# Kernel optimization log

Measured on AMD Instinct MI355X. Metric: run time of the kernel, lower is better.

Reference implementation:

```python
import jax, jax.numpy as jnp
import numpy as np

B, LAT, ADIM, NACT, H = 131072, 64, 16, 9, 128

def setup_inputs() -> dict:
    key = jax.random.key(0)
    ks = jax.random.split(key, 24)
    p = lambda k, shp: (jax.random.normal(k, shp, dtype=jnp.float32) * 0.05)
    return {
        "z_t": jax.random.normal(ks[0], (B, LAT), dtype=jnp.float32),
        "action": jax.random.randint(ks[1], (B,), 0, NACT),
        "hidden": jnp.zeros((1, B, H), dtype=jnp.float32),
        "embed": p(ks[2], (NACT, ADIM)),
        "fuse_W": p(ks[3], (H, LAT + ADIM)), "fuse_b": p(ks[4], (H,)),
        "W_ih": p(ks[5], (3 * H, H)), "W_hh": p(ks[6], (3 * H, H)),
        "b_ih": p(ks[7], (3 * H,)), "b_hh": p(ks[8], (3 * H,)),
        "ns_W1": p(ks[9], (H, H)), "ns_b1": p(ks[10], (H,)),
        "ns_W2": p(ks[11], (LAT, H)), "ns_b2": p(ks[12], (LAT,)),
        "rw_W1": p(ks[13], (H // 2, H)), "rw_b1": p(ks[14], (H // 2,)),
        "rw_W2": p(ks[15], (1, H // 2)), "rw_b2": p(ks[16], (1,)),
        "dn_W1": p(ks[17], (H // 2, H)), "dn_b1": p(ks[18], (H // 2,)),
        "dn_W2": p(ks[19], (1, H // 2)), "dn_b2": p(ks[20], (1,)),
    }

def _mlp2(x, W1, b1, W2, b2):
    return jax.nn.relu(x @ W1.T + b1) @ W2.T + b2

def reference(z_t, action, hidden, embed, fuse_W, fuse_b, W_ih, W_hh, b_ih, b_hh,
              ns_W1, ns_b1, ns_W2, ns_b2, rw_W1, rw_b1, rw_W2, rw_b2,
              dn_W1, dn_b1, dn_W2, dn_b2):
    a_emb = embed[action]                                  # [B, ADIM]
    fused = jnp.concatenate([z_t, a_emb], axis=-1)         # [B, LAT+ADIM]
    x = jax.nn.relu(fused @ fuse_W.T + fuse_b)             # [B, H]
    h0 = hidden[0]                                         # [B, H]
    gi = x @ W_ih.T + b_ih                                 # [B, 3H]
    gh = h0 @ W_hh.T + b_hh                                # [B, 3H]
    Hd = x.shape[-1]
    r = jax.nn.sigmoid(gi[:, :Hd] + gh[:, :Hd])
    zg = jax.nn.sigmoid(gi[:, Hd:2 * Hd] + gh[:, Hd:2 * Hd])
    n = jnp.tanh(gi[:, 2 * Hd:] + r * gh[:, 2 * Hd:])
    h_new = (1.0 - zg) * n + zg * h0                       # [B, H]
    out = h_new
    z_next = _mlp2(out, ns_W1, ns_b1, ns_W2, ns_b2)        # [B, LAT]
    reward = _mlp2(out, rw_W1, rw_b1, rw_W2, rw_b2)        # [B, 1]
    done_logit = _mlp2(out, dn_W1, dn_b1, dn_W2, dn_b2)    # [B, 1]
    return (z_next, reward, done_logit, h_new[None])
```

## Files before the change

### kernel.cpp

```cpp
#include <hip/hip_runtime.h>
#include <cstddef>
#include <cstdint>

#define BATCH 131072
#define HOFF ((size_t)BATCH * 66)

typedef __attribute__((ext_vector_type(8))) short short8;
typedef __attribute__((ext_vector_type(4))) short short4v;
typedef __attribute__((ext_vector_type(4))) float f32x4;

typedef const __attribute__((address_space(1))) unsigned int* gas_t;
typedef __attribute__((address_space(3))) unsigned int* las_t;

#define WS_WF    0
#define WS_GRU   13312
#define WS_HEAD  119808
#define WS_ELEMS 165888

#define MFMA(a,b,c) __builtin_amdgcn_mfma_f32_16x16x32_bf16((a),(b),(c),0,0,0)

__device__ __forceinline__ short f2bf(float x) {
    unsigned u = __builtin_bit_cast(unsigned, x);
    unsigned r = (u + 0x7fffu + ((u >> 16) & 1u)) >> 16;
    return (short)r;
}
__device__ __forceinline__ float bf2f(short s) {
    unsigned u = ((unsigned)(unsigned short)s) << 16;
    return __builtin_bit_cast(float, u);
}
__device__ __forceinline__ float fsigmoid(float x) { return __builtin_amdgcn_rcpf(1.0f + __expf(-x)); }
__device__ __forceinline__ float ftanh(float x)    { return 1.0f - 2.0f * __builtin_amdgcn_rcpf(1.0f + __expf(2.0f * x)); }

__device__ __forceinline__ short8 packbf(f32x4 a, f32x4 b) {
    short8 r;
    r[0]=f2bf(a[0]); r[1]=f2bf(a[1]); r[2]=f2bf(a[2]); r[3]=f2bf(a[3]);
    r[4]=f2bf(b[0]); r[5]=f2bf(b[1]); r[6]=f2bf(b[2]); r[7]=f2bf(b[3]);
    return r;
}

template<int NCH>
__device__ __forceinline__ void stage_lds(const short* __restrict__ src, short* dst, int t) {
    constexpr int NP = (NCH + 255) / 256;
    #pragma unroll
    for (int k = 0; k < NP; ++k) {
        int c = t + 256 * k;
        if ((NCH % 256 == 0) || c < NCH)
            __builtin_amdgcn_global_load_lds((gas_t)(const void*)(src + (size_t)c * 8),
                                             (las_t)(void*)(dst + (size_t)c * 8), 16, 0, 0);
    }
}

extern "C" __global__ void prep_weights(const float* __restrict__ fuse_W,
                                        const float* __restrict__ W_ih, const float* __restrict__ W_hh,
                                        const float* __restrict__ ns_W1, const float* __restrict__ ns_W2,
                                        const float* __restrict__ rw_W1, const float* __restrict__ dn_W1,
                                        short* __restrict__ ws) {
    int i = blockIdx.x * 256 + threadIdx.x;
    if (i >= WS_ELEMS) return;
    float v = 0.f;
    if (i < WS_GRU) {
        int j = i / 104, k = i % 104;
        if (k < 80) v = fuse_W[j*80 + k];
    } else if (i < WS_HEAD) {
        int g = (i - WS_GRU) / 6656, e = (i - WS_GRU) % 6656;
        int r = e / 136, k = e % 136;
        if (r < 48 && k < 128) {
            int j = g >> 1;
            const float* W = (g & 1) ? W_hh : W_ih;
            int gate = r >> 4, rr = r & 15;
            v = W[(size_t)(gate*128 + j*16 + rr)*128 + k];
        }
    } else {
        int h = (i - WS_HEAD) / 4608, e = (i - WS_HEAD) % 4608;
        int r = e / 136, k = e % 136;
        if (r < 32 && k < 128) {
            const float* W; int rb;
            if (h < 4)      { W = ns_W1; rb = h*32; }
            else if (h < 6) { W = ns_W2; rb = (h-4)*32; }
            else if (h < 8) { W = rw_W1; rb = (h-6)*32; }
            else            { W = dn_W1; rb = (h-8)*32; }
            v = W[(size_t)(rb + r)*128 + k];
        }
    }
    ws[i] = f2bf(v);
}

extern "C" __global__ __launch_bounds__(256, 2)
void gru_mfma(const float* __restrict__ z_t, const int* __restrict__ action,
              const float* __restrict__ hidden, const float* __restrict__ embed,
              const float* __restrict__ fuse_b,
              const float* __restrict__ b_ih, const float* __restrict__ b_hh,
              const float* __restrict__ ns_b1, const float* __restrict__ ns_b2,
              const float* __restrict__ rw_b1, const float* __restrict__ rw_W2, const float* __restrict__ rw_b2,
              const float* __restrict__ dn_b1, const float* __restrict__ dn_W2, const float* __restrict__ dn_b2,
              const short* __restrict__ ws, float* __restrict__ out)
{
    __shared__ __align__(16) short smem[30720];

    const int t    = threadIdx.x;
    const int lane = t & 63;
    const int w    = t >> 6;
    const int lo   = lane & 15;
    const int hi   = lane >> 4;
    const int R    = blockIdx.x * 128 + w * 32;
    short* const aw = &smem[13312 + w * 4352];

    const f32x4 zz4 = {0.f, 0.f, 0.f, 0.f};

    stage_lds<1664>(ws, &smem[0], t);

    short8 fa[2][3];
    short8 ha[2][4];
    #pragma unroll
    for (int rt = 0; rt < 2; ++rt) {
        const int row = R + rt*16 + lo;
        #pragma unroll
        for (int kt = 0; kt < 2; ++kt) {
            f32x4 p0 = *(const f32x4*)&z_t[(size_t)row*64 + kt*32 + hi*8];
            f32x4 p1 = *(const f32x4*)&z_t[(size_t)row*64 + kt*32 + hi*8 + 4];
            fa[rt][kt] = packbf(p0, p1);
        }
        if (hi < 2) {
            int a = action[row];
            f32x4 e0 = *(const f32x4*)&embed[a*16 + hi*8];
            f32x4 e1 = *(const f32x4*)&embed[a*16 + hi*8 + 4];
            fa[rt][2] = packbf(e0, e1);
        } else {
            short8 z8 = {0,0,0,0,0,0,0,0};
            fa[rt][2] = z8;
        }
        #pragma unroll
        for (int kt = 0; kt < 4; ++kt) {
            f32x4 p0 = *(const f32x4*)&hidden[(size_t)row*128 + kt*32 + hi*8];
            f32x4 p1 = *(const f32x4*)&hidden[(size_t)row*128 + kt*32 + hi*8 + 4];
            ha[rt][kt] = packbf(p0, p1);
        }
    }

    #pragma unroll
    for (int rt = 0; rt < 2; ++rt)
        #pragma unroll
        for (int kt = 0; kt < 4; ++kt)
            *(short8*)&aw[(rt*16 + lo)*136 + kt*32 + hi*8] = ha[rt][kt];
    unsigned h0d[8][2][2];
    #pragma unroll
    for (int j = 0; j < 8; ++j)
        #pragma unroll
        for (int rt = 0; rt < 2; ++rt)
            #pragma unroll
            for (int p = 0; p < 2; ++p) {
                unsigned a = (unsigned short)aw[(rt*16 + 4*hi + 2*p    )*136 + j*16 + lo];
                unsigned b = (unsigned short)aw[(rt*16 + 4*hi + 2*p + 1)*136 + j*16 + lo];
                h0d[j][rt][p] = a | (b << 16);
            }
    __syncthreads();

    #pragma unroll 1
    for (int ct = 0; ct < 8; ++ct) {
        float fb = fuse_b[ct*16 + lo];
        f32x4 a0 = zz4, a1 = zz4;
        #pragma unroll
        for (int kt = 0; kt < 3; ++kt) {
            short8 B = *(const short8*)&smem[(ct*16 + lo)*104 + kt*32 + hi*8];
            a0 = MFMA(fa[0][kt], B, a0);
            a1 = MFMA(fa[1][kt], B, a1);
        }
        #pragma unroll
        for (int e = 0; e < 4; ++e) {
            aw[(4*hi + e)*136 + ct*16 + lo]        = f2bf(fmaxf(a0[e] + fb, 0.f));
            aw[(16 + 4*hi + e)*136 + ct*16 + lo]   = f2bf(fmaxf(a1[e] + fb, 0.f));
        }
    }
    short8 xa[2][4];
    #pragma unroll
    for (int rt = 0; rt < 2; ++rt)
        #pragma unroll
        for (int kt = 0; kt < 4; ++kt)
            xa[rt][kt] = *(const short8*)&aw[(rt*16 + lo)*136 + kt*32 + hi*8];

    __syncthreads();
    stage_lds<832>(ws + WS_GRU, &smem[0], t);
    __syncthreads();

    f32x4 accI[3][2], accH[3][2];
    #pragma unroll
    for (int j = 0; j < 8; ++j) {
        stage_lds<832>(ws + WS_GRU + (size_t)(2*j + 1) * 6656, &smem[6656], t);
        #pragma unroll
        for (int g = 0; g < 3; ++g) {
            accI[g][0] = zz4; accI[g][1] = zz4;
            #pragma unroll
            for (int kt = 0; kt < 4; ++kt) {
                short8 B = *(const short8*)&smem[(g*16 + lo)*136 + kt*32 + hi*8];
                accI[g][0] = MFMA(xa[0][kt], B, accI[g][0]);
                accI[g][1] = MFMA(xa[1][kt], B, accI[g][1]);
            }
        }
        __syncthreads();

        if (j < 7) stage_lds<832>(ws + WS_GRU + (size_t)(2*j + 2) * 6656, &smem[0], t);
        else       stage_lds<576>(ws + WS_HEAD, &smem[0], t);
        #pragma unroll
        for (int g = 0; g < 3; ++g) {
            accH[g][0] = zz4; accH[g][1] = zz4;
            #pragma unroll
            for (int kt = 0; kt < 4; ++kt) {
                short8 B = *(const short8*)&smem[6656 + (g*16 + lo)*136 + kt*32 + hi*8];
                accH[g][0] = MFMA(ha[0][kt], B, accH[g][0]);
                accH[g][1] = MFMA(ha[1][kt], B, accH[g][1]);
            }
        }
        {
            const int j0 = j * 16;
            const float bir = b_ih[j0+lo], biz = b_ih[128+j0+lo], bin = b_ih[256+j0+lo];
            const float bhr = b_hh[j0+lo], bhz = b_hh[128+j0+lo], bhn = b_hh[256+j0+lo];
            #pragma unroll
            for (int rt = 0; rt < 2; ++rt) {
                #pragma unroll
                for (int p = 0; p < 2; ++p) {
                    unsigned hp = h0d[j][rt][p];
                    float h0a = bf2f((short)(hp & 0xffffu));
                    float h0b = bf2f((short)(hp >> 16));
                    int e = 2*p;
                    {
                        float rg = fsigmoid(accI[0][rt][e] + bir + accH[0][rt][e] + bhr);
                        float zg = fsigmoid(accI[1][rt][e] + biz + accH[1][rt][e] + bhz);
                        float ng = ftanh(accI[2][rt][e] + bin + rg*(accH[2][rt][e] + bhn));
                        aw[(rt*16 + 4*hi + e)*136 + j0 + lo] = f2bf((1.f - zg)*ng + zg*h0a);
                    }
                    {
                        float rg = fsigmoid(accI[0][rt][e+1] + bir + accH[0][rt][e+1] + bhr);
                        float zg = fsigmoid(accI[1][rt][e+1] + biz + accH[1][rt][e+1] + bhz);
                        float ng = ftanh(accI[2][rt][e+1] + bin + rg*(accH[2][rt][e+1] + bhn));
                        aw[(rt*16 + 4*hi + e+1)*136 + j0 + lo] = f2bf((1.f - zg)*ng + zg*h0b);
                    }
                }
            }
        }
        __syncthreads();
    }

    short8 hfa[2][4], ta[2][4];
    #pragma unroll 1
    for (int u = 16; u < 26; ++u) {
        if (u < 25)
            stage_lds<576>(ws + WS_HEAD + (size_t)(u - 15) * 4608, &smem[((u+1)&1)*6656], t);
        const int halfB = (u & 1) * 6656;

        if (u == 16) {
            #pragma unroll 1
            for (int i = 0; i < 16; ++i) {
                int v = i*64 + lane;
                int row = v >> 5, col = (v & 31) * 4;
                short4v s = *(const short4v*)&aw[row*136 + col];
                f32x4 f = { bf2f(s[0]), bf2f(s[1]), bf2f(s[2]), bf2f(s[3]) };
                *(f32x4*)&out[HOFF + (size_t)(R + row)*128 + col] = f;
            }
            #pragma unroll
            for (int rt = 0; rt < 2; ++rt)
                #pragma unroll
                for (int kt = 0; kt < 4; ++kt)
                    hfa[rt][kt] = *(const short8*)&aw[(rt*16 + lo)*136 + kt*32 + hi*8];
        }
        if (u == 20) {
            #pragma unroll
            for (int rt = 0; rt < 2; ++rt)
                #pragma unroll
                for (int kt = 0; kt < 4; ++kt)
                    ta[rt][kt] = *(const short8*)&aw[(rt*16 + lo)*136 + kt*32 + hi*8];
        }

        if (u < 20) {
            const int uh = u - 16;
            #pragma unroll
            for (int sub = 0; sub < 2; ++sub) {
                const int j0 = (uh*2 + sub) * 16;
                float b1 = ns_b1[j0 + lo];
                f32x4 a0 = zz4, a1 = zz4;
                #pragma unroll
                for (int kt = 0; kt < 4; ++kt) {
                    short8 B = *(const short8*)&smem[halfB + (sub*16 + lo)*136 + kt*32 + hi*8];
                    a0 = MFMA(hfa[0][kt], B, a0);
                    a1 = MFMA(hfa[1][kt], B, a1);
                }
                #pragma unroll
                for (int e = 0; e < 4; ++e) {
                    aw[(4*hi + e)*136 + j0 + lo]      = f2bf(fmaxf(a0[e] + b1, 0.f));
                    aw[(16 + 4*hi + e)*136 + j0 + lo] = f2bf(fmaxf(a1[e] + b1, 0.f));
                }
            }
        } else if (u < 22) {
            const int uh = u - 20;
            #pragma unroll
            for (int sub = 0; sub < 2; ++sub) {
                const int j0 = (uh*2 + sub) * 16;
                float b2 = ns_b2[j0 + lo];
                f32x4 a0 = zz4, a1 = zz4;
                #pragma unroll
                for (int kt = 0; kt < 4; ++kt) {
                    short8 B = *(const short8*)&smem[halfB + (sub*16 + lo)*136 + kt*32 + hi*8];
                    a0 = MFMA(ta[0][kt], B, a0);
                    a1 = MFMA(ta[1][kt], B, a1);
                }
                #pragma unroll
                for (int e = 0; e < 4; ++e) {
                    aw[(4*hi + e)*72 + j0 + lo]      = f2bf(a0[e] + b2);
                    aw[(16 + 4*hi + e)*72 + j0 + lo] = f2bf(a1[e] + b2);
                }
            }
            if (u == 21) {
                #pragma unroll 1
                for (int i = 0; i < 8; ++i) {
                    int v = i*64 + lane;
                    int row = v >> 4, col = (v & 15) * 4;
                    short4v s = *(const short4v*)&aw[row*72 + col];
                    f32x4 f = { bf2f(s[0]), bf2f(s[1]), bf2f(s[2]), bf2f(s[3]) };
                    *(f32x4*)&out[(size_t)(R + row)*64 + col] = f;
                }
            }
        } else if (u < 24) {
            const int uh = u - 22;
            #pragma unroll
            for (int sub = 0; sub < 2; ++sub) {
                const int j0 = (uh*2 + sub) * 16;
                float b1 = rw_b1[j0 + lo];
                f32x4 a0 = zz4, a1 = zz4;
                #pragma unroll
                for (int kt = 0; kt < 4; ++kt) {
                    short8 B = *(const short8*)&smem[halfB + (sub*16 + lo)*136 + kt*32 + hi*8];
                    a0 = MFMA(hfa[0][kt], B, a0);
                    a1 = MFMA(hfa[1][kt], B, a1);
                }
                #pragma unroll
                for (int e = 0; e < 4; ++e) {
                    aw[(4*hi + e)*136 + j0 + lo]      = f2bf(fmaxf(a0[e] + b1, 0.f));
                    aw[(16 + 4*hi + e)*136 + j0 + lo] = f2bf(fmaxf(a1[e] + b1, 0.f));
                }
            }
        } else {
            const int uh = u - 24;
            #pragma unroll
            for (int sub = 0; sub < 2; ++sub) {
                const int j0 = (uh*2 + sub) * 16;
                float b1 = dn_b1[j0 + lo];
                f32x4 a0 = zz4, a1 = zz4;
                #pragma unroll
                for (int kt = 0; kt < 4; ++kt) {
                    short8 B = *(const short8*)&smem[halfB + (sub*16 + lo)*136 + kt*32 + hi*8];
                    a0 = MFMA(hfa[0][kt], B, a0);
                    a1 = MFMA(hfa[1][kt], B, a1);
                }
                #pragma unroll
                for (int e = 0; e < 4; ++e) {
                    aw[(4*hi + e)*136 + 64 + j0 + lo]      = f2bf(fmaxf(a0[e] + b1, 0.f));
                    aw[(16 + 4*hi + e)*136 + 64 + j0 + lo] = f2bf(fmaxf(a1[e] + b1, 0.f));
                }
            }
        }
        __syncthreads();
    }

    {
        const float* W2   = (lane < 32) ? rw_W2 : dn_W2;
        float acc         = (lane < 32) ? rw_b2[0] : dn_b2[0];
        const int colbase = (lane < 32) ? 0 : 64;
        const int rr      = lane & 31;
        #pragma unroll
        for (int k = 0; k < 64; k += 4) {
            short4v s = *(const short4v*)&aw[rr*136 + colbase + k];
            f32x4 wv  = *(const f32x4*)&W2[k];
            acc += bf2f(s[0])*wv[0] + bf2f(s[1])*wv[1] + bf2f(s[2])*wv[2] + bf2f(s[3])*wv[3];
        }
        size_t ooff = (lane < 32) ? ((size_t)BATCH*64) : ((size_t)BATCH*65);
        out[ooff + R + rr] = acc;
    }
}

extern "C" void kernel_launch(void* const* d_in, const int* in_sizes, int n_in,
                              void* d_out, int out_size, void* d_ws, size_t ws_size,
                              hipStream_t stream) {
    const float* z_t    = (const float*)d_in[0];
    const int*   action = (const int*)  d_in[1];
    const float* hidden = (const float*)d_in[2];
    const float* embed  = (const float*)d_in[3];
    const float* fuse_W = (const float*)d_in[4];
    const float* fuse_b = (const float*)d_in[5];
    const float* W_ih   = (const float*)d_in[6];
    const float* W_hh   = (const float*)d_in[7];
    const float* b_ih   = (const float*)d_in[8];
    const float* b_hh   = (const float*)d_in[9];
    const float* ns_W1  = (const float*)d_in[10];
    const float* ns_b1  = (const float*)d_in[11];
    const float* ns_W2  = (const float*)d_in[12];
    const float* ns_b2  = (const float*)d_in[13];
    const float* rw_W1  = (const float*)d_in[14];
    const float* rw_b1  = (const float*)d_in[15];
    const float* rw_W2  = (const float*)d_in[16];
    const float* rw_b2  = (const float*)d_in[17];
    const float* dn_W1  = (const float*)d_in[18];
    const float* dn_b1  = (const float*)d_in[19];
    const float* dn_W2  = (const float*)d_in[20];
    const float* dn_b2  = (const float*)d_in[21];
    float* out = (float*)d_out;
    short* ws  = (short*)d_ws;

    hipLaunchKernelGGL(prep_weights, dim3((WS_ELEMS + 255) / 256), dim3(256), 0, stream,
                       fuse_W, W_ih, W_hh, ns_W1, ns_W2, rw_W1, dn_W1, ws);

    hipLaunchKernelGGL(gru_mfma, dim3(BATCH / 128), dim3(256), 0, stream,
                       z_t, action, hidden, embed,
                       fuse_b, b_ih, b_hh, ns_b1, ns_b2,
                       rw_b1, rw_W2, rw_b2, dn_b1, dn_W2, dn_b2,
                       ws, out);
}
```

Measured before the change: 92.99 us.

## Double block size, shrink per-wave LDS scratch, and interleave output stores with compute

Blocks grow from 256 to 512 threads (8 waves, 256 rows), and launch bounds request 4 blocks per CU. Each wave's LDS scratch shrinks from a 136-wide row buffer to two 40-wide strip buffers, so more waves fit and each staged weight tile serves more rows. Stores of h_new are spread across the GRU loop, the fuse layer is split so weight staging overlaps compute, and the head stage loop is unrolled into explicit steps with the scalar heads computed from strips. The cost is higher register pressure under the tighter launch bound, and two of the h_new fragments are reloaded from global output memory.

After: 128.3 us. 1.38x slower.

```diff
diff --git a/kernel.cpp b/kernel.cpp
--- a/kernel.cpp
+++ b/kernel.cpp
@@ -12,7 +12,6 @@
 typedef const __attribute__((address_space(1))) unsigned int* gas_t;
 typedef __attribute__((address_space(3))) unsigned int* las_t;
 
-#define WS_WF    0
 #define WS_GRU   13312
 #define WS_HEAD  119808
 #define WS_ELEMS 165888
@@ -40,11 +39,11 @@
 
 template<int NCH>
 __device__ __forceinline__ void stage_lds(const short* __restrict__ src, short* dst, int t) {
-    constexpr int NP = (NCH + 255) / 256;
+    constexpr int NP = (NCH + 511) / 512;
     #pragma unroll
     for (int k = 0; k < NP; ++k) {
-        int c = t + 256 * k;
-        if ((NCH % 256 == 0) || c < NCH)
+        int c = t + 512 * k;
+        if ((NCH % 512 == 0) || c < NCH)
             __builtin_amdgcn_global_load_lds((gas_t)(const void*)(src + (size_t)c * 8),
                                              (las_t)(void*)(dst + (size_t)c * 8), 16, 0, 0);
     }
@@ -85,7 +84,25 @@
     ws[i] = f2bf(v);
 }
 
-extern "C" __global__ __launch_bounds__(256, 2)
+#define HEAD_GEMM(FRAG, BIAS, Q, HALFOFF, SP, RELU) do {                                   \
+    _Pragma("unroll") for (int sub = 0; sub < 2; ++sub) {                                  \
+        float bb = (BIAS)[(Q)*32 + sub*16 + lo];                                           \
+        f32x4 a0 = zz4, a1 = zz4;                                                          \
+        _Pragma("unroll") for (int kt = 0; kt < 4; ++kt) {                                 \
+            short8 Bf = *(const short8*)&smem[(HALFOFF) + (sub*16+lo)*136 + kt*32 + hi*8]; \
+            a0 = MFMA((FRAG)[0][kt], Bf, a0); a1 = MFMA((FRAG)[1][kt], Bf, a1); }          \
+        _Pragma("unroll") for (int e = 0; e < 4; ++e) {                                    \
+            float v0 = a0[e] + bb, v1 = a1[e] + bb;                                        \
+            if (RELU) { v0 = fmaxf(v0, 0.f); v1 = fmaxf(v1, 0.f); }                        \
+            (SP)[(4*hi+e)*40 + sub*16 + lo]      = f2bf(v0);                               \
+            (SP)[(16+4*hi+e)*40 + sub*16 + lo]   = f2bf(v1); }                             \
+    } } while (0)
+
+#define TA_READ(Q, SP) do {                                            \
+    ta[0][Q] = *(const short8*)&(SP)[lo*40 + hi*8];                    \
+    ta[1][Q] = *(const short8*)&(SP)[(16+lo)*40 + hi*8]; } while (0)
+
+extern "C" __global__ __launch_bounds__(512, 4)
 void gru_mfma(const float* __restrict__ z_t, const int* __restrict__ action,
               const float* __restrict__ hidden, const float* __restrict__ embed,
               const float* __restrict__ fuse_b,
@@ -93,19 +110,55 @@
               const float* __restrict__ ns_b1, const float* __restrict__ ns_b2,
               const float* __restrict__ rw_b1, const float* __restrict__ rw_W2, const float* __restrict__ rw_b2,
               const float* __restrict__ dn_b1, const float* __restrict__ dn_W2, const float* __restrict__ dn_b2,
-              const short* __restrict__ ws, float* __restrict__ out)
+              const short* __restrict__ ws, float* out)
 {
-    __shared__ __align__(16) short smem[30720];
+    __shared__ __align__(16) short smem[33792];
 
     const int t    = threadIdx.x;
     const int lane = t & 63;
     const int w    = t >> 6;
     const int lo   = lane & 15;
     const int hi   = lane >> 4;
-    const int R    = blockIdx.x * 128 + w * 32;
-    short* const aw = &smem[13312 + w * 4352];
+    const int R    = blockIdx.x * 256 + w * 32;
+    short* const S0 = &smem[13312 + w * 2560];
+    short* const S1 = S0 + 1280;
 
     const f32x4 zz4 = {0.f, 0.f, 0.f, 0.f};
+
+    auto store_hnew_strip = [&](const short* SP, int kt) {
+        #pragma unroll
+        for (int v = 0; v < 4; ++v) {
+            int idx = v*64 + lane;
+            int r = idx >> 3, c = (idx & 7) * 4;
+            short4v s = *(const short4v*)&SP[r*40 + c];
+            f32x4 f = { bf2f(s[0]), bf2f(s[1]), bf2f(s[2]), bf2f(s[3]) };
+            *(f32x4*)&out[HOFF + (size_t)(R + r)*128 + kt*32 + c] = f;
+        }
+    };
+    auto store_z_strip = [&](const short* SP, int q) {
+        #pragma unroll
+        for (int v = 0; v < 4; ++v) {
+            int idx = v*64 + lane;
+            int r = idx >> 3, c = (idx & 7) * 4;
+            short4v s = *(const short4v*)&SP[r*40 + c];
+            f32x4 f = { bf2f(s[0]), bf2f(s[1]), bf2f(s[2]), bf2f(s[3]) };
+            *(f32x4*)&out[(size_t)(R + r)*64 + q*32 + c] = f;
+        }
+    };
+    auto head1_dot = [&](const float* W2, float b2) -> float {
+        int rr = lane & 31;
+        float acc = b2;
+        #pragma unroll
+        for (int kk = 0; kk < 64; kk += 8) {
+            const short* SP = (kk < 32) ? S0 : S1;
+            short8 s = *(const short8*)&SP[rr*40 + (kk & 31)];
+            f32x4 w0 = *(const f32x4*)&W2[kk];
+            f32x4 w1 = *(const f32x4*)&W2[kk+4];
+            acc += bf2f(s[0])*w0[0] + bf2f(s[1])*w0[1] + bf2f(s[2])*w0[2] + bf2f(s[3])*w0[3]
+                 + bf2f(s[4])*w1[0] + bf2f(s[5])*w1[1] + bf2f(s[6])*w1[2] + bf2f(s[7])*w1[3];
+        }
+        return acc;
+    };
 
     stage_lds<1664>(ws, &smem[0], t);
 
@@ -136,56 +189,90 @@
             ha[rt][kt] = packbf(p0, p1);
         }
     }
-
-    #pragma unroll
-    for (int rt = 0; rt < 2; ++rt)
-        #pragma unroll
-        for (int kt = 0; kt < 4; ++kt)
-            *(short8*)&aw[(rt*16 + lo)*136 + kt*32 + hi*8] = ha[rt][kt];
+    float fbv[8];
+    #pragma unroll
+    for (int ct = 0; ct < 8; ++ct) fbv[ct] = fuse_b[ct*16 + lo];
+
     unsigned h0d[8][2][2];
     #pragma unroll
-    for (int j = 0; j < 8; ++j)
-        #pragma unroll
-        for (int rt = 0; rt < 2; ++rt)
-            #pragma unroll
-            for (int p = 0; p < 2; ++p) {
-                unsigned a = (unsigned short)aw[(rt*16 + 4*hi + 2*p    )*136 + j*16 + lo];
-                unsigned b = (unsigned short)aw[(rt*16 + 4*hi + 2*p + 1)*136 + j*16 + lo];
-                h0d[j][rt][p] = a | (b << 16);
-            }
-    __syncthreads();
-
-    #pragma unroll 1
-    for (int ct = 0; ct < 8; ++ct) {
-        float fb = fuse_b[ct*16 + lo];
-        f32x4 a0 = zz4, a1 = zz4;
-        #pragma unroll
-        for (int kt = 0; kt < 3; ++kt) {
-            short8 B = *(const short8*)&smem[(ct*16 + lo)*104 + kt*32 + hi*8];
-            a0 = MFMA(fa[0][kt], B, a0);
-            a1 = MFMA(fa[1][kt], B, a1);
-        }
-        #pragma unroll
-        for (int e = 0; e < 4; ++e) {
-            aw[(4*hi + e)*136 + ct*16 + lo]        = f2bf(fmaxf(a0[e] + fb, 0.f));
-            aw[(16 + 4*hi + e)*136 + ct*16 + lo]   = f2bf(fmaxf(a1[e] + fb, 0.f));
-        }
-    }
+    for (int kt = 0; kt < 4; ++kt) {
+        short* SP = (kt & 1) ? S1 : S0;
+        *(short8*)&SP[lo*40 + hi*8]        = ha[0][kt];
+        *(short8*)&SP[(16 + lo)*40 + hi*8] = ha[1][kt];
+        #pragma unroll
+        for (int c = 0; c < 2; ++c) {
+            int j = 2*kt + c;
+            #pragma unroll
+            for (int rt = 0; rt < 2; ++rt)
+                #pragma unroll
+                for (int p = 0; p < 2; ++p) {
+                    unsigned a = (unsigned short)SP[(rt*16 + 4*hi + 2*p    )*40 + c*16 + lo];
+                    unsigned b = (unsigned short)SP[(rt*16 + 4*hi + 2*p + 1)*40 + c*16 + lo];
+                    h0d[j][rt][p] = a | (b << 16);
+                }
+        }
+    }
+    __syncthreads();
+
     short8 xa[2][4];
     #pragma unroll
-    for (int rt = 0; rt < 2; ++rt)
-        #pragma unroll
-        for (int kt = 0; kt < 4; ++kt)
-            xa[rt][kt] = *(const short8*)&aw[(rt*16 + lo)*136 + kt*32 + hi*8];
-
+    for (int kt = 0; kt < 2; ++kt) {
+        short* SP = (kt & 1) ? S1 : S0;
+        #pragma unroll
+        for (int c = 0; c < 2; ++c) {
+            int ct = kt*2 + c;
+            f32x4 a0 = zz4, a1 = zz4;
+            #pragma unroll
+            for (int fk = 0; fk < 3; ++fk) {
+                short8 B = *(const short8*)&smem[(ct*16 + lo)*104 + fk*32 + hi*8];
+                a0 = MFMA(fa[0][fk], B, a0);
+                a1 = MFMA(fa[1][fk], B, a1);
+            }
+            #pragma unroll
+            for (int e = 0; e < 4; ++e) {
+                SP[(4*hi + e)*40 + c*16 + lo]      = f2bf(fmaxf(a0[e] + fbv[ct], 0.f));
+                SP[(16 + 4*hi + e)*40 + c*16 + lo] = f2bf(fmaxf(a1[e] + fbv[ct], 0.f));
+            }
+        }
+        xa[0][kt] = *(const short8*)&SP[lo*40 + hi*8];
+        xa[1][kt] = *(const short8*)&SP[(16 + lo)*40 + hi*8];
+    }
     __syncthreads();
     stage_lds<832>(ws + WS_GRU, &smem[0], t);
-    __syncthreads();
-
-    f32x4 accI[3][2], accH[3][2];
+
+    #pragma unroll
+    for (int kt = 2; kt < 4; ++kt) {
+        short* SP = (kt & 1) ? S1 : S0;
+        #pragma unroll
+        for (int c = 0; c < 2; ++c) {
+            int ct = kt*2 + c;
+            f32x4 a0 = zz4, a1 = zz4;
+            #pragma unroll
+            for (int fk = 0; fk < 3; ++fk) {
+                short8 B = *(const short8*)&smem[6656 + ((ct - 4)*16 + lo)*104 + fk*32 + hi*8];
+                a0 = MFMA(fa[0][fk], B, a0);
+                a1 = MFMA(fa[1][fk], B, a1);
+            }
+            #pragma unroll
+            for (int e = 0; e < 4; ++e) {
+                SP[(4*hi + e)*40 + c*16 + lo]      = f2bf(fmaxf(a0[e] + fbv[ct], 0.f));
+                SP[(16 + 4*hi + e)*40 + c*16 + lo] = f2bf(fmaxf(a1[e] + fbv[ct], 0.f));
+            }
+        }
+        xa[0][kt] = *(const short8*)&SP[lo*40 + hi*8];
+        xa[1][kt] = *(const short8*)&SP[(16 + lo)*40 + hi*8];
+    }
+    __syncthreads();
+
     #pragma unroll
     for (int j = 0; j < 8; ++j) {
-        stage_lds<832>(ws + WS_GRU + (size_t)(2*j + 1) * 6656, &smem[6656], t);
+        stage_lds<832>(ws + WS_GRU + (size_t)(2*j + 1)*6656, &smem[6656], t);
+        if (j == 2) store_hnew_strip(S0, 0);
+        if (j == 4) store_hnew_strip(S1, 1);
+        const int j0 = j * 16;
+        const float bir = b_ih[j0+lo], biz = b_ih[128+j0+lo], bin = b_ih[256+j0+lo];
+        const float bhr = b_hh[j0+lo], bhz = b_hh[128+j0+lo], bhn = b_hh[256+j0+lo];
+        f32x4 accI[3][2];
         #pragma unroll
         for (int g = 0; g < 3; ++g) {
             accI[g][0] = zz4; accI[g][1] = zz4;
@@ -198,8 +285,9 @@
         }
         __syncthreads();
 
-        if (j < 7) stage_lds<832>(ws + WS_GRU + (size_t)(2*j + 2) * 6656, &smem[0], t);
+        if (j < 7) stage_lds<832>(ws + WS_GRU + (size_t)(2*j + 2)*6656, &smem[0], t);
         else       stage_lds<576>(ws + WS_HEAD, &smem[0], t);
+        f32x4 accH[3][2];
         #pragma unroll
         for (int g = 0; g < 3; ++g) {
             accH[g][0] = zz4; accH[g][1] = zz4;
@@ -211,9 +299,7 @@
             }
         }
         {
-            const int j0 = j * 16;
-            const float bir = b_ih[j0+lo], biz = b_ih[128+j0+lo], bin = b_ih[256+j0+lo];
-            const float bhr = b_hh[j0+lo], bhz = b_hh[128+j0+lo], bhn = b_hh[256+j0+lo];
+            short* HP = ((j >> 1) & 1) ? S1 : S0;
             #pragma unroll
             for (int rt = 0; rt < 2; ++rt) {
                 #pragma unroll
@@ -226,13 +312,13 @@
                         float rg = fsigmoid(accI[0][rt][e] + bir + accH[0][rt][e] + bhr);
                         float zg = fsigmoid(accI[1][rt][e] + biz + accH[1][rt][e] + bhz);
                         float ng = ftanh(accI[2][rt][e] + bin + rg*(accH[2][rt][e] + bhn));
-                        aw[(rt*16 + 4*hi + e)*136 + j0 + lo] = f2bf((1.f - zg)*ng + zg*h0a);
+                        HP[(rt*16 + 4*hi + e)*40 + (j&1)*16 + lo] = f2bf((1.f - zg)*ng + zg*h0a);
                     }
                     {
                         float rg = fsigmoid(accI[0][rt][e+1] + bir + accH[0][rt][e+1] + bhr);
                         float zg = fsigmoid(accI[1][rt][e+1] + biz + accH[1][rt][e+1] + bhz);
                         float ng = ftanh(accI[2][rt][e+1] + bin + rg*(accH[2][rt][e+1] + bhn));
-                        aw[(rt*16 + 4*hi + e+1)*136 + j0 + lo] = f2bf((1.f - zg)*ng + zg*h0b);
+                        HP[(rt*16 + 4*hi + e+1)*40 + (j&1)*16 + lo] = f2bf((1.f - zg)*ng + zg*h0b);
                     }
                 }
             }
@@ -241,138 +327,72 @@
     }
 
     short8 hfa[2][4], ta[2][4];
-    #pragma unroll 1
-    for (int u = 16; u < 26; ++u) {
-        if (u < 25)
-            stage_lds<576>(ws + WS_HEAD + (size_t)(u - 15) * 4608, &smem[((u+1)&1)*6656], t);
-        const int halfB = (u & 1) * 6656;
-
-        if (u == 16) {
-            #pragma unroll 1
-            for (int i = 0; i < 16; ++i) {
-                int v = i*64 + lane;
-                int row = v >> 5, col = (v & 31) * 4;
-                short4v s = *(const short4v*)&aw[row*136 + col];
-                f32x4 f = { bf2f(s[0]), bf2f(s[1]), bf2f(s[2]), bf2f(s[3]) };
-                *(f32x4*)&out[HOFF + (size_t)(R + row)*128 + col] = f;
-            }
-            #pragma unroll
-            for (int rt = 0; rt < 2; ++rt)
-                #pragma unroll
-                for (int kt = 0; kt < 4; ++kt)
-                    hfa[rt][kt] = *(const short8*)&aw[(rt*16 + lo)*136 + kt*32 + hi*8];
-        }
-        if (u == 20) {
-            #pragma unroll
-            for (int rt = 0; rt < 2; ++rt)
-                #pragma unroll
-                for (int kt = 0; kt < 4; ++kt)
-                    ta[rt][kt] = *(const short8*)&aw[(rt*16 + lo)*136 + kt*32 + hi*8];
-        }
-
-        if (u < 20) {
-            const int uh = u - 16;
-            #pragma unroll
-            for (int sub = 0; sub < 2; ++sub) {
-                const int j0 = (uh*2 + sub) * 16;
-                float b1 = ns_b1[j0 + lo];
-                f32x4 a0 = zz4, a1 = zz4;
-                #pragma unroll
-                for (int kt = 0; kt < 4; ++kt) {
-                    short8 B = *(const short8*)&smem[halfB + (sub*16 + lo)*136 + kt*32 + hi*8];
-                    a0 = MFMA(hfa[0][kt], B, a0);
-                    a1 = MFMA(hfa[1][kt], B, a1);
-                }
-                #pragma unroll
-                for (int e = 0; e < 4; ++e) {
-                    aw[(4*hi + e)*136 + j0 + lo]      = f2bf(fmaxf(a0[e] + b1, 0.f));
-                    aw[(16 + 4*hi + e)*136 + j0 + lo] = f2bf(fmaxf(a1[e] + b1, 0.f));
-                }
-            }
-        } else if (u < 22) {
-            const int uh = u - 20;
-            #pragma unroll
-            for (int sub = 0; sub < 2; ++sub) {
-                const int j0 = (uh*2 + sub) * 16;
-                float b2 = ns_b2[j0 + lo];
-                f32x4 a0 = zz4, a1 = zz4;
-                #pragma unroll
-                for (int kt = 0; kt < 4; ++kt) {
-                    short8 B = *(const short8*)&smem[halfB + (sub*16 + lo)*136 + kt*32 + hi*8];
-                    a0 = MFMA(ta[0][kt], B, a0);
-                    a1 = MFMA(ta[1][kt], B, a1);
-                }
-                #pragma unroll
-                for (int e = 0; e < 4; ++e) {
-                    aw[(4*hi + e)*72 + j0 + lo]      = f2bf(a0[e] + b2);
-                    aw[(16 + 4*hi + e)*72 + j0 + lo] = f2bf(a1[e] + b2);
-                }
-            }
-            if (u == 21) {
-                #pragma unroll 1
-                for (int i = 0; i < 8; ++i) {
-                    int v = i*64 + lane;
-                    int row = v >> 4, col = (v & 15) * 4;
-                    short4v s = *(const short4v*)&aw[row*72 + col];
-                    f32x4 f = { bf2f(s[0]), bf2f(s[1]), bf2f(s[2]), bf2f(s[3]) };
-                    *(f32x4*)&out[(size_t)(R + row)*64 + col] = f;
-                }
-            }
-        } else if (u < 24) {
-            const int uh = u - 22;
-            #pragma unroll
-            for (int sub = 0; sub < 2; ++sub) {
-                const int j0 = (uh*2 + sub) * 16;
-                float b1 = rw_b1[j0 + lo];
-                f32x4 a0 = zz4, a1 = zz4;
-                #pragma unroll
-                for (int kt = 0; kt < 4; ++kt) {
-                    short8 B = *(const short8*)&smem[halfB + (sub*16 + lo)*136 + kt*32 + hi*8];
-                    a0 = MFMA(hfa[0][kt], B, a0);
-                    a1 = MFMA(hfa[1][kt], B, a1);
-                }
-                #pragma unroll
-                for (int e = 0; e < 4; ++e) {
-                    aw[(4*hi + e)*136 + j0 + lo]      = f2bf(fmaxf(a0[e] + b1, 0.f));
-                    aw[(16 + 4*hi + e)*136 + j0 + lo] = f2bf(fmaxf(a1[e] + b1, 0.f));
-                }
-            }
-        } else {
-            const int uh = u - 24;
-            #pragma unroll
-            for (int sub = 0; sub < 2; ++sub) {
-                const int j0 = (uh*2 + sub) * 16;
-                float b1 = dn_b1[j0 + lo];
-                f32x4 a0 = zz4, a1 = zz4;
-                #pragma unroll
-                for (int kt = 0; kt < 4; ++kt) {
-                    short8 B = *(const short8*)&smem[halfB + (sub*16 + lo)*136 + kt*32 + hi*8];
-                    a0 = MFMA(hfa[0][kt], B, a0);
-                    a1 = MFMA(hfa[1][kt], B, a1);
-                }
-                #pragma unroll
-                for (int e = 0; e < 4; ++e) {
-                    aw[(4*hi + e)*136 + 64 + j0 + lo]      = f2bf(fmaxf(a0[e] + b1, 0.f));
-                    aw[(16 + 4*hi + e)*136 + 64 + j0 + lo] = f2bf(fmaxf(a1[e] + b1, 0.f));
-                }
-            }
-        }
-        __syncthreads();
-    }
-
+
+    stage_lds<576>(ws + WS_HEAD + 4608, &smem[6656], t);
+    store_hnew_strip(S0, 2);
+    store_hnew_strip(S1, 3);
+    hfa[0][2] = *(const short8*)&S0[lo*40 + hi*8];
+    hfa[1][2] = *(const short8*)&S0[(16+lo)*40 + hi*8];
+    hfa[0][3] = *(const short8*)&S1[lo*40 + hi*8];
+    hfa[1][3] = *(const short8*)&S1[(16+lo)*40 + hi*8];
+    #pragma unroll
+    for (int rt = 0; rt < 2; ++rt)
+        #pragma unroll
+        for (int kt = 0; kt < 2; ++kt) {
+            const float* p = &out[HOFF + (size_t)(R + rt*16 + lo)*128 + kt*32 + hi*8];
+            f32x4 p0 = *(const f32x4*)p;
+            f32x4 p1 = *(const f32x4*)(p + 4);
+            hfa[rt][kt] = packbf(p0, p1);
+        }
+    HEAD_GEMM(hfa, ns_b1, 0, 0, S0, true);
+    TA_READ(0, S0);
+    __syncthreads();
+
+    stage_lds<576>(ws + WS_HEAD + 2*4608, &smem[0], t);
+    HEAD_GEMM(hfa, ns_b1, 1, 6656, S1, true);
+    TA_READ(1, S1);
+    __syncthreads();
+
+    stage_lds<576>(ws + WS_HEAD + 3*4608, &smem[6656], t);
+    HEAD_GEMM(hfa, ns_b1, 2, 0, S0, true);
+    TA_READ(2, S0);
+    __syncthreads();
+
+    stage_lds<576>(ws + WS_HEAD + 4*4608, &smem[0], t);
+    HEAD_GEMM(hfa, ns_b1, 3, 6656, S1, true);
+    TA_READ(3, S1);
+    __syncthreads();
+
+    stage_lds<576>(ws + WS_HEAD + 5*4608, &smem[6656], t);
+    HEAD_GEMM(ta, ns_b2, 0, 0, S0, false);
+    store_z_strip(S0, 0);
+    __syncthreads();
+
+    stage_lds<576>(ws + WS_HEAD + 6*4608, &smem[0], t);
+    HEAD_GEMM(ta, ns_b2, 1, 6656, S1, false);
+    store_z_strip(S1, 1);
+    __syncthreads();
+
+    stage_lds<576>(ws + WS_HEAD + 7*4608, &smem[6656], t);
+    HEAD_GEMM(hfa, rw_b1, 0, 0, S0, true);
+    __syncthreads();
+
+    stage_lds<576>(ws + WS_HEAD + 8*4608, &smem[0], t);
+    HEAD_GEMM(hfa, rw_b1, 1, 6656, S1, true);
+    __syncthreads();
+
+    stage_lds<576>(ws + WS_HEAD + 9*4608, &smem[6656], t);
     {
-        const float* W2   = (lane < 32) ? rw_W2 : dn_W2;
-        float acc         = (lane < 32) ? rw_b2[0] : dn_b2[0];
-        const int colbase = (lane < 32) ? 0 : 64;
-        const int rr      = lane & 31;
-        #pragma unroll
-        for (int k = 0; k < 64; k += 4) {
-            short4v s = *(const short4v*)&aw[rr*136 + colbase + k];
-            f32x4 wv  = *(const f32x4*)&W2[k];
-            acc += bf2f(s[0])*wv[0] + bf2f(s[1])*wv[1] + bf2f(s[2])*wv[2] + bf2f(s[3])*wv[3];
-        }
-        size_t ooff = (lane < 32) ? ((size_t)BATCH*64) : ((size_t)BATCH*65);
-        out[ooff + R + rr] = acc;
+        float racc = head1_dot(rw_W2, rw_b2[0]);
+        if (lane < 32) out[(size_t)BATCH*64 + R + (lane & 31)] = racc;
+    }
+    HEAD_GEMM(hfa, dn_b1, 0, 0, S0, true);
+    __syncthreads();
+
+    HEAD_GEMM(hfa, dn_b1, 1, 6656, S1, true);
+    {
+        float dacc = head1_dot(dn_W2, dn_b2[0]);
+        if (lane < 32) out[(size_t)BATCH*65 + R + (lane & 31)] = dacc;
     }
 }
 
@@ -407,7 +427,7 @@
     hipLaunchKernelGGL(prep_weights, dim3((WS_ELEMS + 255) / 256), dim3(256), 0, stream,
                        fuse_W, W_ih, W_hh, ns_W1, ns_W2, rw_W1, dn_W1, ws);
 
-    hipLaunchKernelGGL(gru_mfma, dim3(BATCH / 128), dim3(256), 0, stream,
+    hipLaunchKernelGGL(gru_mfma, dim3(BATCH / 256), dim3(512), 0, stream,
                        z_t, action, hidden, embed,
                        fuse_b, b_ih, b_hh, ns_b1, ns_b2,
                        rw_b1, rw_W2, rw_b2, dn_b1, dn_W2, dn_b2,
```
